# Kernel tuning notes

Measured on AMD Instinct MI355X. Metric: run time of the kernel, lower is better.

## Reference

```python
import jax, jax.numpy as jnp
import numpy as np

B, T, V, D, H, L, NFF, K = 16, 256, 30000, 512, 256, 2, 2, 20
# D = input_size = hidden_size (required by residual in FeedForwardNet); H = hidden_size//2 per LSTM direction


def _lstm_dir(x, Wih, Whh, b, reverse):
    # x: [B,T,Din]; Wih: [4H,Din]; Whh: [4H,H]; b: [4H] (b_ih + b_hh)
    Bq = x.shape[0]
    Hd = Whh.shape[1]
    if reverse:
        x = x[:, ::-1]
    xw = jnp.einsum('bti,gi->btg', x, Wih) + b  # [B,T,4H]

    def step(carry, xw_t):
        h, c = carry
        g = xw_t + h @ Whh.T
        i, f, gg, o = jnp.split(g, 4, axis=-1)  # torch gate order i,f,g,o
        c = jax.nn.sigmoid(f) * c + jax.nn.sigmoid(i) * jnp.tanh(gg)
        h = jax.nn.sigmoid(o) * jnp.tanh(c)
        return (h, c), h

    h0 = jnp.zeros((Bq, Hd), x.dtype)
    _, hs = jax.lax.scan(step, (h0, h0), jnp.swapaxes(xw, 0, 1))
    hs = jnp.swapaxes(hs, 0, 1)  # [B,T,H]
    if reverse:
        hs = hs[:, ::-1]
    return hs


def _bilstm(x, Wih, Whh, b):
    # Wih: [L,2,4H,Din], Whh: [L,2,4H,H], b: [L,2,4H]; Din = 2H = D for all layers
    h = x
    for l in range(L):
        fwd = _lstm_dir(h, Wih[l, 0], Whh[l, 0], b[l, 0], False)
        bwd = _lstm_dir(h, Wih[l, 1], Whh[l, 1], b[l, 1], True)
        h = jnp.concatenate([fwd, bwd], axis=-1)  # [B,T,2H]
    return h


def _viterbi(em, start, end, trans):
    # em: [B,T,K] emissions, full mask; torchcrf Viterbi decode
    Bq, Tq, Kq = em.shape
    score = start + em[:, 0]  # [B,K]

    def step(score, em_t):
        bs = score[:, :, None] + trans[None] + em_t[:, None, :]  # [B,K,K]
        return jnp.max(bs, axis=1), jnp.argmax(bs, axis=1)

    score, hist = jax.lax.scan(step, score, jnp.swapaxes(em[:, 1:], 0, 1))  # hist [T-1,B,K]
    best = jnp.argmax(score + end, axis=-1)  # [B]

    def back(tag, h_t):
        prev = jnp.take_along_axis(h_t, tag[:, None], axis=1)[:, 0]
        return prev, prev

    _, prevs = jax.lax.scan(back, best, hist, reverse=True)  # [T-1,B]
    return jnp.concatenate([prevs, best[None]], axis=0).T  # [B,T]


def setup_inputs() -> dict:
    key = jax.random.key(0)
    ks = jax.random.split(key, 16)
    s = 0.05
    inp = {
        'x': jax.random.randint(ks[0], (B, T), 0, V),
        'emb': jax.random.normal(ks[1], (V, D), jnp.float32) * s,
        'lstm_Wih': jax.random.normal(ks[2], (L, 2, 4 * H, D), jnp.float32) * s,
        'lstm_Whh': jax.random.normal(ks[3], (L, 2, 4 * H, H), jnp.float32) * s,
        'lstm_b': jax.random.normal(ks[4], (L, 2, 4 * H), jnp.float32) * s,
        'ff_W1': jax.random.normal(ks[5], (NFF, D, D), jnp.float32) * s,
        'ff_b1': jax.random.normal(ks[6], (NFF, D), jnp.float32) * s,
        'ff_W2': jax.random.normal(ks[7], (NFF, D, D), jnp.float32) * s,
        'ff_b2': jax.random.normal(ks[8], (NFF, D), jnp.float32) * s,
        'ffo_W': jax.random.normal(ks[9], (H, D), jnp.float32) * s,
        'ffo_b': jax.random.normal(ks[10], (H,), jnp.float32) * s,
        'out_W': jax.random.normal(ks[11], (K, H), jnp.float32) * s,
        'out_b': jax.random.normal(ks[12], (K,), jnp.float32) * s,
        'crf_start': jax.random.normal(ks[13], (K,), jnp.float32) * 0.1,
        'crf_end': jax.random.normal(ks[14], (K,), jnp.float32) * 0.1,
        'crf_trans': jax.random.normal(ks[15], (K, K), jnp.float32) * 0.1,
    }
    return inp


def reference(x, emb, lstm_Wih, lstm_Whh, lstm_b, ff_W1, ff_b1, ff_W2, ff_b2,
              ffo_W, ffo_b, out_W, out_b, crf_start, crf_end, crf_trans):
    h = emb[x]                       # [B,T,D] frozen embedding lookup
    h = _bilstm(h, lstm_Wih, lstm_Whh, lstm_b)  # [B,T,D] (2H == D)
    res = h
    for n in range(NFF):             # residual MLP stack (dropout = identity in eval)
        h = jax.nn.relu(h @ ff_W1[n].T + ff_b1[n]) @ ff_W2[n].T + ff_b2[n]
    h = h + res
    h = h @ ffo_W.T + ffo_b          # [B,T,H] FeedForwardNet.output
    em = h @ out_W.T + out_b         # [B,T,K] emissions
    tag = _viterbi(em, crf_start, crf_end, crf_trans)  # [B,T] int32
    return em, tag
```

## Files before the change

kernel.cpp:

```cpp
#include <hip/hip_runtime.h>
#include <hip/hip_bf16.h>
#include <stdint.h>

typedef unsigned short u16;
typedef unsigned int   u32;
typedef __attribute__((ext_vector_type(4))) float f32x4;
typedef __attribute__((ext_vector_type(8))) short bf16x8;

static __device__ __forceinline__ u16 f2bf(float x) {
  union { float f; u32 u; } v; v.f = x;
  u32 r = v.u + 0x7FFFu + ((v.u >> 16) & 1u);
  return (u16)(r >> 16);
}
static __device__ __forceinline__ float bf2f(u16 b) {
  union { u32 u; float f; } v; v.u = ((u32)b) << 16;
  return v.f;
}


__global__ void split_hl(const float* __restrict__ in, u16* __restrict__ hi,
                         u16* __restrict__ lo, int n) {
  int i = blockIdx.x * 256 + threadIdx.x;
  if (i < n) {
    float v = in[i];
    u16 h = f2bf(v);
    hi[i] = h;
    lo[i] = f2bf(v - bf2f(h));
  }
}

__global__ void embed_split(const int* __restrict__ x, const float* __restrict__ emb,
                            u16* __restrict__ hi, u16* __restrict__ lo) {
  int gid = blockIdx.x * 256 + threadIdx.x;
  int bt = gid >> 9, d = gid & 511;
  float v = emb[(size_t)x[bt] * 512 + d];
  u16 h = f2bf(v);
  hi[gid] = h;
  lo[gid] = f2bf(v - bf2f(h));
}

__global__ void lstm_wpack(const float* __restrict__ Whh, u32* __restrict__ wp) {
  int tid = blockIdx.x * 256 + threadIdx.x;
  int dw   = tid & 3;
  int lane = (tid >> 2) & 63;
  int kt   = (tid >> 8) & 7;
  int g    = (tid >> 11) & 3;
  int W    = (tid >> 13) & 15;
  int d    = (tid >> 17) & 1;
  int lyr  = (tid >> 18) & 1;
  int row = g * 256 + W * 16 + (lane & 15);
  int k   = kt * 32 + (lane >> 4) * 8 + dw * 2;
  const float* src = Whh + (((size_t)(lyr * 2 + d) * 1024 + row) * 256);
  u16 h0 = f2bf(src[k]), h1 = f2bf(src[k + 1]);
  wp[tid] = (u32)h0 | ((u32)h1 << 16);
}

__global__ void resadd_split(const float* __restrict__ a, const float* __restrict__ b,
                             u16* __restrict__ hi, u16* __restrict__ lo, int n) {
  int i = blockIdx.x * 256 + threadIdx.x;
  if (i < n) {
    float v = a[i] + b[i];
    u16 h = f2bf(v);
    hi[i] = h;
    lo[i] = f2bf(v - bf2f(h));
  }
}

template<int RELU, int WF32, int WHL, int XSWZ, int BLO>
__global__ __launch_bounds__(256) void gemm_x3(
    const u16* __restrict__ Ahi, const u16* __restrict__ Alo,
    const u16* __restrict__ Bhi, const u16* __restrict__ Blo,
    const float* __restrict__ bias,
    float* __restrict__ Cf, u16* __restrict__ Chi, u16* __restrict__ Clo,
    int M, int N, int Kd)
{
  __shared__ u16 As_hi[128][40], As_lo[128][40], Bs_hi[128][40];
  __shared__ u16 Bs_lo[BLO ? 128 : 1][BLO ? 40 : 1];
  int t = threadIdx.x;
  int bm = blockIdx.x * 128, bn = blockIdx.y * 128;
  int l = t & 63, wid = t >> 6;
  int wy = wid >> 1, wx = wid & 1;
  f32x4 acc[4][4];
#pragma unroll
  for (int i = 0; i < 4; i++)
#pragma unroll
    for (int j = 0; j < 4; j++) acc[i][j] = (f32x4){0.f, 0.f, 0.f, 0.f};

  for (int kt = 0; kt < Kd; kt += 32) {
    __syncthreads();
#pragma unroll
    for (int cc = 0; cc < 2; cc++) {
      int c = t + cc * 256;
      int row = c >> 2, k8 = (c & 3) << 3;
      *(uint4*)&As_hi[row][k8] = *(const uint4*)(Ahi + (size_t)(bm + row) * Kd + kt + k8);
      *(uint4*)&As_lo[row][k8] = *(const uint4*)(Alo + (size_t)(bm + row) * Kd + kt + k8);
      *(uint4*)&Bs_hi[row][k8] = *(const uint4*)(Bhi + (size_t)(bn + row) * Kd + kt + k8);
      if (BLO)
        *(uint4*)&Bs_lo[row][k8] = *(const uint4*)(Blo + (size_t)(bn + row) * Kd + kt + k8);
    }
    __syncthreads();
    bf16x8 bh[4], bl[4];
    int k8 = (l >> 4) << 3;
#pragma unroll
    for (int ni = 0; ni < 4; ni++) {
      int r = wx * 64 + ni * 16 + (l & 15);
      bh[ni] = *(const bf16x8*)&Bs_hi[r][k8];
      if (BLO) bl[ni] = *(const bf16x8*)&Bs_lo[r][k8];
    }
#pragma unroll
    for (int mi = 0; mi < 4; mi++) {
      int r = wy * 64 + mi * 16 + (l & 15);
      bf16x8 ah = *(const bf16x8*)&As_hi[r][k8];
      bf16x8 al = *(const bf16x8*)&As_lo[r][k8];
#pragma unroll
      for (int ni = 0; ni < 4; ni++) {
        acc[mi][ni] = __builtin_amdgcn_mfma_f32_16x16x32_bf16(ah, bh[ni], acc[mi][ni], 0, 0, 0);
        acc[mi][ni] = __builtin_amdgcn_mfma_f32_16x16x32_bf16(al, bh[ni], acc[mi][ni], 0, 0, 0);
        if (BLO)
          acc[mi][ni] = __builtin_amdgcn_mfma_f32_16x16x32_bf16(ah, bl[ni], acc[mi][ni], 0, 0, 0);
      }
    }
  }
#pragma unroll
  for (int ni = 0; ni < 4; ni++) {
    int col = bn + wx * 64 + ni * 16 + (l & 15);
    float bv = bias ? bias[col] : 0.f;
#pragma unroll
    for (int mi = 0; mi < 4; mi++) {
#pragma unroll
      for (int r = 0; r < 4; r++) {
        int row = bm + wy * 64 + mi * 16 + (l >> 4) * 4 + r;
        float v = acc[mi][ni][r] + bv;
        if (RELU) v = fmaxf(v, 0.f);
        if (XSWZ) {
          int tt = row & 255, b = row >> 8;
          int g = col >> 8, c8 = col & 255;
          int Wv = c8 >> 4, uu = c8 & 15;
          int lane = ((b >> 2) << 4) | uu;
          size_t o = ((((size_t)tt * 16 + Wv) * 4 + g) * 64 + lane) * 4 + (b & 3);
          Cf[o] = v;
        } else {
          size_t o = (size_t)row * N + col;
          if (WF32) Cf[o] = v;
          if (WHL) { u16 h = f2bf(v); Chi[o] = h; Clo[o] = f2bf(v - bf2f(h)); }
        }
      }
    }
  }
}

__global__ __launch_bounds__(1024, 1) void lstm_rec3(
    const u32* __restrict__ wpack_l,
    const float* __restrict__ xwsw_f, const float* __restrict__ xwsw_b,
    u16* __restrict__ out_hi, u16* __restrict__ out_lo, float* __restrict__ out_f)
{
  int dir = blockIdx.x;
  int tid = threadIdx.x;
  int W = tid >> 6, l = tid & 63;
  int bb  = l & 15;
  int mb  = (l >> 4) * 4;
  int wu  = W * 16 + (l & 15);
  const float* xw = dir ? xwsw_b : xwsw_f;

  bf16x8 wf[4][8];
#pragma unroll
  for (int g = 0; g < 4; g++) {
    const u32* wb = wpack_l + (size_t)((dir * 16 + W) * 4 + g) * 2048;
#pragma unroll
    for (int kt = 0; kt < 8; kt++)
      wf[g][kt] = *(const bf16x8*)(const void*)(wb + (kt * 64 + l) * 4);
  }

  __shared__ u16 hH[2][16][256];

  f32x4 cst = (f32x4){0.f, 0.f, 0.f, 0.f};

  for (int s = 0; s < 256; s++) {
    int tpos = dir ? (255 - s) : s;
    int cb = s & 1, pb = cb ^ 1;

    const float* xb = xw + ((size_t)tpos * 16 + W) * 1024;
    f32x4 xwv[4];
#pragma unroll
    for (int g = 0; g < 4; g++)
      xwv[g] = *(const f32x4*)(xb + g * 256 + l * 4);

    f32x4 acc[4];
#pragma unroll
    for (int g = 0; g < 4; g++) acc[g] = (f32x4){0.f, 0.f, 0.f, 0.f};

    if (s > 0) {
#pragma unroll
      for (int kt = 0; kt < 8; kt++) {
        int bx = (((kt * 4 + (l >> 4)) ^ (bb & 7)) << 3);
        bf16x8 ah = *(const bf16x8*)&hH[pb][bb][bx];
#pragma unroll
        for (int g = 0; g < 4; g++)
          acc[g] = __builtin_amdgcn_mfma_f32_16x16x32_bf16(ah, wf[g][kt], acc[g], 0, 0, 0);
      }
    }

#pragma unroll
    for (int r = 0; r < 4; r++) {
      float gi = acc[0][r] + xwv[0][r];
      float gf = acc[1][r] + xwv[1][r];
      float gg = acc[2][r] + xwv[2][r];
      float go = acc[3][r] + xwv[3][r];
      float si = 1.f / (1.f + __expf(-gi));
      float sf = 1.f / (1.f + __expf(-gf));
      float so = 1.f / (1.f + __expf(-go));
      float tg = 1.f - 2.f / (__expf(2.f * gg) + 1.f);
      float c = sf * cst[r] + si * tg;
      cst[r] = c;
      float th = 1.f - 2.f / (__expf(2.f * c) + 1.f);
      float h = so * th;

      u16 hb = f2bf(h);
      u16 lb = f2bf(h - bf2f(hb));
      int b = mb + r;
      int idx = ((((wu >> 3) ^ (b & 7)) << 3)) + (wu & 7);
      hH[cb][b][idx] = hb;
      size_t oo = (((size_t)b * 256 + tpos) * 512) + dir * 256 + wu;
      out_hi[oo] = hb;
      out_lo[oo] = lb;
      if (out_f) out_f[oo] = h;
    }
    __syncthreads();
  }
}

__global__ __launch_bounds__(256) void out_gemm(const float* __restrict__ h,
                                                const float* __restrict__ Wo,
                                                const float* __restrict__ bo,
                                                float* __restrict__ em)
{
  int t = threadIdx.x;
  if (t >= 160) return;
  int r = t / 20, j = t - r * 20;
  int bt = blockIdx.x * 8 + r;
  const float* hr = h + (size_t)bt * 256;
  const float* wr = Wo + j * 256;
  float acc = 0.f;
#pragma unroll 4
  for (int k = 0; k < 256; k++) acc += hr[k] * wr[k];
  em[(size_t)bt * 20 + j] = acc + bo[j];
}

__global__ __launch_bounds__(192) void viterbi(const float* __restrict__ em,
                                               const float* __restrict__ cstart,
                                               const float* __restrict__ cend,
                                               const float* __restrict__ ctrans,
                                               float* __restrict__ tago)
{
  __shared__ float sc[8][20];
  __shared__ float tl[400];
  __shared__ unsigned char hist[255][8][20];
  int t = threadIdx.x;
  for (int i = t; i < 400; i += 192) tl[i] = ctrans[i];
  int bl = t / 20, j = t - bl * 20;
  bool act = (t < 160);
  int b = blockIdx.x * 8 + bl;
  if (act) sc[bl][j] = cstart[j] + em[((size_t)b * 256) * 20 + j];
  __syncthreads();
  for (int step = 1; step < 256; step++) {
    float best = -1e30f; int bi = 0;
    if (act) {
      best = sc[bl][0] + tl[j]; bi = 0;
#pragma unroll
      for (int i = 1; i < 20; i++) {
        float v = sc[bl][i] + tl[i * 20 + j];
        if (v > best) { best = v; bi = i; }
      }
      hist[step - 1][bl][j] = (unsigned char)bi;
    }
    __syncthreads();
    if (act) sc[bl][j] = best + em[((size_t)b * 256 + step) * 20 + j];
    __syncthreads();
  }
  if (act && j == 0) {
    float best = sc[bl][0] + cend[0]; int bj = 0;
    for (int i = 1; i < 20; i++) {
      float v = sc[bl][i] + cend[i];
      if (v > best) { best = v; bj = i; }
    }
    int tag = bj;
    tago[(size_t)b * 256 + 255] = (float)tag;
    for (int step = 254; step >= 0; step--) {
      tag = hist[step][bl][tag];
      tago[(size_t)b * 256 + step] = (float)tag;
    }
  }
}

extern "C" void kernel_launch(void* const* d_in, const int* in_sizes, int n_in,
                              void* d_out, int out_size, void* d_ws, size_t ws_size,
                              hipStream_t stream)
{
  const int*   x   = (const int*)  d_in[0];
  const float* emb = (const float*)d_in[1];
  const float* Wih = (const float*)d_in[2];
  const float* Whh = (const float*)d_in[3];
  const float* lb  = (const float*)d_in[4];
  const float* fW1 = (const float*)d_in[5];
  const float* fb1 = (const float*)d_in[6];
  const float* fW2 = (const float*)d_in[7];
  const float* fb2 = (const float*)d_in[8];
  const float* foW = (const float*)d_in[9];
  const float* fob = (const float*)d_in[10];
  const float* oW  = (const float*)d_in[11];
  const float* ob  = (const float*)d_in[12];
  const float* cst = (const float*)d_in[13];
  const float* cen = (const float*)d_in[14];
  const float* ctr = (const float*)d_in[15];

  const size_t MB = 1u << 20;
  if (ws_size < 100 * MB) return;
  char* ws = (char*)d_ws;

  u16* embHi = (u16*)(ws + 0 * MB);
  u16* embLo = (u16*)(ws + 4 * MB);
  u16* l1Hi  = (u16*)(ws + 8 * MB);
  u16* l1Lo  = (u16*)(ws + 12 * MB);
  float* l2F = (float*)(ws + 16 * MB);
  u16* l2Hi  = (u16*)(ws + 24 * MB);
  u16* l2Lo  = (u16*)(ws + 28 * MB);
  float* xwF = (float*)(ws + 32 * MB);
  float* xwB = (float*)(ws + 48 * MB);
  u32* wpck  = (u32*)(ws + 80 * MB);
  u16* wihHi = (u16*)(ws + 84 * MB);
  u16* wihLo = (u16*)(ws + 88 * MB);
  u16* fw1Hi = (u16*)(ws + 92 * MB);
  u16* fw1Lo = (u16*)(ws + 93 * MB);
  u16* fw2Hi = (u16*)(ws + 94 * MB);
  u16* fw2Lo = (u16*)(ws + 95 * MB);
  u16* ffoHi = (u16*)(ws + 96 * MB);
  u16* ffoLo = (u16*)(ws + 96 * MB + 512 * 1024);
  u16* t1Hi = (u16*)xwF;
  u16* t1Lo = (u16*)((char*)xwF + 4 * MB);
  u16* t2Hi = (u16*)xwB;
  u16* t2Lo = (u16*)((char*)xwB + 4 * MB);
  float* h2F = (float*)((char*)xwB + 8 * MB);
  u16* sumHi = (u16*)((char*)xwF + 8 * MB);
  u16* sumLo = (u16*)((char*)xwF + 12 * MB);
  float* h256F = (float*)xwF;

  float* em   = (float*)d_out;
  float* tago = (float*)d_out + 81920;

  dim3 blk(256);

  split_hl<<<8192, blk, 0, stream>>>(Wih, wihHi, wihLo, 4 * 1024 * 512);
  split_hl<<<2048, blk, 0, stream>>>(fW1, fw1Hi, fw1Lo, 2 * 512 * 512);
  split_hl<<<2048, blk, 0, stream>>>(fW2, fw2Hi, fw2Lo, 2 * 512 * 512);
  split_hl<<<512,  blk, 0, stream>>>(foW, ffoHi, ffoLo, 256 * 512);
  lstm_wpack<<<2048, blk, 0, stream>>>(Whh, wpck);
  embed_split<<<8192, blk, 0, stream>>>(x, emb, embHi, embLo);

  gemm_x3<0,1,0,1,0><<<dim3(32, 8), blk, 0, stream>>>(embHi, embLo,
      wihHi + 0 * 524288, wihLo + 0 * 524288, lb + 0 * 1024,
      xwF, nullptr, nullptr, 4096, 1024, 512);
  gemm_x3<0,1,0,1,0><<<dim3(32, 8), blk, 0, stream>>>(embHi, embLo,
      wihHi + 1 * 524288, wihLo + 1 * 524288, lb + 1 * 1024,
      xwB, nullptr, nullptr, 4096, 1024, 512);
  lstm_rec3<<<2, dim3(1024), 0, stream>>>(wpck, xwF, xwB, l1Hi, l1Lo, nullptr);

  gemm_x3<0,1,0,1,0><<<dim3(32, 8), blk, 0, stream>>>(l1Hi, l1Lo,
      wihHi + 2 * 524288, wihLo + 2 * 524288, lb + 2 * 1024,
      xwF, nullptr, nullptr, 4096, 1024, 512);
  gemm_x3<0,1,0,1,0><<<dim3(32, 8), blk, 0, stream>>>(l1Hi, l1Lo,
      wihHi + 3 * 524288, wihLo + 3 * 524288, lb + 3 * 1024,
      xwB, nullptr, nullptr, 4096, 1024, 512);
  lstm_rec3<<<2, dim3(1024), 0, stream>>>(wpck + 262144, xwF, xwB,
      l2Hi, l2Lo, l2F);

  gemm_x3<1,0,1,0,0><<<dim3(32, 4), blk, 0, stream>>>(l2Hi, l2Lo,
      fw1Hi + 0, fw1Lo + 0, fb1 + 0, nullptr, t1Hi, t1Lo, 4096, 512, 512);
  gemm_x3<0,0,1,0,0><<<dim3(32, 4), blk, 0, stream>>>(t1Hi, t1Lo,
      fw2Hi + 0, fw2Lo + 0, fb2 + 0, nullptr, t2Hi, t2Lo, 4096, 512, 512);
  gemm_x3<1,0,1,0,0><<<dim3(32, 4), blk, 0, stream>>>(t2Hi, t2Lo,
      fw1Hi + 262144, fw1Lo + 262144, fb1 + 512, nullptr, t1Hi, t1Lo, 4096, 512, 512);
  gemm_x3<0,1,0,0,0><<<dim3(32, 4), blk, 0, stream>>>(t1Hi, t1Lo,
      fw2Hi + 262144, fw2Lo + 262144, fb2 + 512, h2F, nullptr, nullptr, 4096, 512, 512);
  resadd_split<<<8192, blk, 0, stream>>>(h2F, l2F, sumHi, sumLo, 4096 * 512);
  gemm_x3<0,1,0,0,0><<<dim3(32, 2), blk, 0, stream>>>(sumHi, sumLo,
      ffoHi, ffoLo, fob, h256F, nullptr, nullptr, 4096, 256, 512);

  out_gemm<<<512, blk, 0, stream>>>(h256F, oW, ob, em);
  viterbi<<<2, dim3(192), 0, stream>>>(em, cst, cen, ctr, tago);
}
```

Measured before the change: 6.236 ms.

## Run LSTM recurrence in fp8 with a two-pass bf16 weight-residual correction

The recurrent matmul now uses fp8 MFMA with fp8-packed Whh held in registers, and 512-thread blocks each cover 32 hidden units. A first pass runs the recurrence to get approximate h. A parallel bf16 GEMM then multiplies those h values by the fp8 quantization residual of Whh, and a second fp8 pass adds that correction and also carries an fp8 hi/lo split of h. The aim is to shorten the serial per-step critical path. In exchange each layer runs the recurrence twice plus extra GEMMs, and accuracy depends on the correction from the first-pass h being close enough.

```diff
diff --git a/kernel.cpp b/kernel.cpp
--- a/kernel.cpp
+++ b/kernel.cpp
@@ -6,6 +6,7 @@
 typedef unsigned int   u32;
 typedef __attribute__((ext_vector_type(4))) float f32x4;
 typedef __attribute__((ext_vector_type(8))) short bf16x8;
+typedef __attribute__((ext_vector_type(4))) unsigned short u16x4;
 
 static __device__ __forceinline__ u16 f2bf(float x) {
   union { float f; u32 u; } v; v.f = x;
@@ -39,42 +40,53 @@
   lo[gid] = f2bf(v - bf2f(h));
 }
 
-__global__ void lstm_wpack(const float* __restrict__ Whh, u32* __restrict__ wp) {
+__global__ void lstm_wpack_fp8(const float* __restrict__ Whh, u32* __restrict__ wp,
+                               u16* __restrict__ dW) {
   int tid = blockIdx.x * 256 + threadIdx.x;
-  int dw   = tid & 3;
-  int lane = (tid >> 2) & 63;
-  int kt   = (tid >> 8) & 7;
+  int dw   = tid & 1;
+  int lane = (tid >> 1) & 63;
+  int kt   = (tid >> 7) & 7;
+  int ni   = (tid >> 10) & 1;
   int g    = (tid >> 11) & 3;
-  int W    = (tid >> 13) & 15;
-  int d    = (tid >> 17) & 1;
-  int lyr  = (tid >> 18) & 1;
-  int row = g * 256 + W * 16 + (lane & 15);
-  int k   = kt * 32 + (lane >> 4) * 8 + dw * 2;
-  const float* src = Whh + (((size_t)(lyr * 2 + d) * 1024 + row) * 256);
-  u16 h0 = f2bf(src[k]), h1 = f2bf(src[k + 1]);
-  wp[tid] = (u32)h0 | ((u32)h1 << 16);
-}
-
-__global__ void resadd_split(const float* __restrict__ a, const float* __restrict__ b,
+  int W    = (tid >> 13) & 7;
+  int dir  = (tid >> 16) & 1;
+  int lyr  = (tid >> 17) & 1;
+  int row = g * 256 + W * 32 + ni * 16 + (lane & 15);
+  int k   = kt * 32 + (lane >> 4) * 8 + dw * 4;
+  int ld = lyr * 2 + dir;
+  const float* src = Whh + (((size_t)ld * 1024 + row) * 256);
+  u32 v = __builtin_amdgcn_cvt_pk_fp8_f32(src[k], src[k + 1], 0, 0);
+  v = __builtin_amdgcn_cvt_pk_fp8_f32(src[k + 2], src[k + 3], v, 1);
+  wp[tid] = v;
+  u16* dst = dW + ((size_t)ld * 1024 + row) * 256 + k;
+  dst[0] = f2bf(src[k]     - __builtin_amdgcn_cvt_f32_fp8((int)v, 0));
+  dst[1] = f2bf(src[k + 1] - __builtin_amdgcn_cvt_f32_fp8((int)v, 1));
+  dst[2] = f2bf(src[k + 2] - __builtin_amdgcn_cvt_f32_fp8((int)v, 2));
+  dst[3] = f2bf(src[k + 3] - __builtin_amdgcn_cvt_f32_fp8((int)v, 3));
+}
+
+__global__ void resadd_split(const float* __restrict__ a, const u16* __restrict__ bHi,
+                             const u16* __restrict__ bLo,
                              u16* __restrict__ hi, u16* __restrict__ lo, int n) {
   int i = blockIdx.x * 256 + threadIdx.x;
   if (i < n) {
-    float v = a[i] + b[i];
+    float v = a[i] + bf2f(bHi[i]) + bf2f(bLo[i]);
     u16 h = f2bf(v);
     hi[i] = h;
     lo[i] = f2bf(v - bf2f(h));
   }
 }
 
-template<int RELU, int WF32, int WHL, int XSWZ, int BLO>
+template<int RELU, int WF32, int WHL, int XSWZ, int BLO, int ALO>
 __global__ __launch_bounds__(256) void gemm_x3(
     const u16* __restrict__ Ahi, const u16* __restrict__ Alo,
     const u16* __restrict__ Bhi, const u16* __restrict__ Blo,
     const float* __restrict__ bias,
     float* __restrict__ Cf, u16* __restrict__ Chi, u16* __restrict__ Clo,
-    int M, int N, int Kd)
+    int M, int N, int Kd, int lda)
 {
-  __shared__ u16 As_hi[128][40], As_lo[128][40], Bs_hi[128][40];
+  __shared__ u16 As_hi[128][40], Bs_hi[128][40];
+  __shared__ u16 As_lo[ALO ? 128 : 1][ALO ? 40 : 1];
   __shared__ u16 Bs_lo[BLO ? 128 : 1][BLO ? 40 : 1];
   int t = threadIdx.x;
   int bm = blockIdx.x * 128, bn = blockIdx.y * 128;
@@ -92,8 +104,9 @@
     for (int cc = 0; cc < 2; cc++) {
       int c = t + cc * 256;
       int row = c >> 2, k8 = (c & 3) << 3;
-      *(uint4*)&As_hi[row][k8] = *(const uint4*)(Ahi + (size_t)(bm + row) * Kd + kt + k8);
-      *(uint4*)&As_lo[row][k8] = *(const uint4*)(Alo + (size_t)(bm + row) * Kd + kt + k8);
+      *(uint4*)&As_hi[row][k8] = *(const uint4*)(Ahi + (size_t)(bm + row) * lda + kt + k8);
+      if (ALO)
+        *(uint4*)&As_lo[row][k8] = *(const uint4*)(Alo + (size_t)(bm + row) * lda + kt + k8);
       *(uint4*)&Bs_hi[row][k8] = *(const uint4*)(Bhi + (size_t)(bn + row) * Kd + kt + k8);
       if (BLO)
         *(uint4*)&Bs_lo[row][k8] = *(const uint4*)(Blo + (size_t)(bn + row) * Kd + kt + k8);
@@ -111,11 +124,13 @@
     for (int mi = 0; mi < 4; mi++) {
       int r = wy * 64 + mi * 16 + (l & 15);
       bf16x8 ah = *(const bf16x8*)&As_hi[r][k8];
-      bf16x8 al = *(const bf16x8*)&As_lo[r][k8];
+      bf16x8 al;
+      if (ALO) al = *(const bf16x8*)&As_lo[r][k8];
 #pragma unroll
       for (int ni = 0; ni < 4; ni++) {
         acc[mi][ni] = __builtin_amdgcn_mfma_f32_16x16x32_bf16(ah, bh[ni], acc[mi][ni], 0, 0, 0);
-        acc[mi][ni] = __builtin_amdgcn_mfma_f32_16x16x32_bf16(al, bh[ni], acc[mi][ni], 0, 0, 0);
+        if (ALO)
+          acc[mi][ni] = __builtin_amdgcn_mfma_f32_16x16x32_bf16(al, bh[ni], acc[mi][ni], 0, 0, 0);
         if (BLO)
           acc[mi][ni] = __builtin_amdgcn_mfma_f32_16x16x32_bf16(ah, bl[ni], acc[mi][ni], 0, 0, 0);
       }
@@ -134,11 +149,12 @@
         if (RELU) v = fmaxf(v, 0.f);
         if (XSWZ) {
           int tt = row & 255, b = row >> 8;
-          int g = col >> 8, c8 = col & 255;
-          int Wv = c8 >> 4, uu = c8 & 15;
+          int g = col >> 8, u8 = col & 255;
+          int Wv = u8 >> 5, nn = (u8 >> 4) & 1, uu = u8 & 15;
           int lane = ((b >> 2) << 4) | uu;
-          size_t o = ((((size_t)tt * 16 + Wv) * 4 + g) * 64 + lane) * 4 + (b & 3);
-          Cf[o] = v;
+          size_t o = ((((((size_t)tt * 8 + Wv) * 4 + g) * 2 + nn) * 64) + lane) * 4 + (b & 3);
+          if (WHL) Chi[o] = f2bf(v);
+          else Cf[o] = v;
         } else {
           size_t o = (size_t)row * N + col;
           if (WF32) Cf[o] = v;
@@ -149,81 +165,122 @@
   }
 }
 
-__global__ __launch_bounds__(1024, 1) void lstm_rec3(
+template<int PASS>
+__global__ __launch_bounds__(512, 2) void lstm_rec5(
     const u32* __restrict__ wpack_l,
     const float* __restrict__ xwsw_f, const float* __restrict__ xwsw_b,
-    u16* __restrict__ out_hi, u16* __restrict__ out_lo, float* __restrict__ out_f)
+    const u16* __restrict__ corr_f, const u16* __restrict__ corr_b,
+    u16* __restrict__ h1out,
+    u16* __restrict__ out_hi, u16* __restrict__ out_lo)
 {
   int dir = blockIdx.x;
   int tid = threadIdx.x;
   int W = tid >> 6, l = tid & 63;
   int bb  = l & 15;
   int mb  = (l >> 4) * 4;
-  int wu  = W * 16 + (l & 15);
   const float* xw = dir ? xwsw_b : xwsw_f;
-
-  bf16x8 wf[4][8];
-#pragma unroll
-  for (int g = 0; g < 4; g++) {
-    const u32* wb = wpack_l + (size_t)((dir * 16 + W) * 4 + g) * 2048;
-#pragma unroll
-    for (int kt = 0; kt < 8; kt++)
-      wf[g][kt] = *(const bf16x8*)(const void*)(wb + (kt * 64 + l) * 4);
-  }
-
-  __shared__ u16 hH[2][16][256];
-
-  f32x4 cst = (f32x4){0.f, 0.f, 0.f, 0.f};
+  const u16* corr = dir ? corr_b : corr_f;
+
+  long wf[4][2][8];
+  {
+    const long* wp64 = (const long*)wpack_l;
+#pragma unroll
+    for (int g = 0; g < 4; g++)
+#pragma unroll
+      for (int ni = 0; ni < 2; ni++)
+#pragma unroll
+        for (int kt = 0; kt < 8; kt++)
+          wf[g][ni][kt] = wp64[(size_t)((((dir * 8 + W) * 4 + g) * 2 + ni) * 8 + kt) * 64 + l];
+  }
+
+  __shared__ unsigned char hH8[2][16][256];
+  __shared__ unsigned char hL8[PASS == 2 ? 2 : 1][PASS == 2 ? 16 : 1][PASS == 2 ? 256 : 1];
+
+  f32x4 cst[2] = {(f32x4){0.f,0.f,0.f,0.f}, (f32x4){0.f,0.f,0.f,0.f}};
 
   for (int s = 0; s < 256; s++) {
     int tpos = dir ? (255 - s) : s;
     int cb = s & 1, pb = cb ^ 1;
 
-    const float* xb = xw + ((size_t)tpos * 16 + W) * 1024;
-    f32x4 xwv[4];
+    const float* xb = xw + ((size_t)tpos * 8 + W) * 2048;
+    f32x4 acc[4][2];
 #pragma unroll
     for (int g = 0; g < 4; g++)
-      xwv[g] = *(const f32x4*)(xb + g * 256 + l * 4);
-
-    f32x4 acc[4];
-#pragma unroll
-    for (int g = 0; g < 4; g++) acc[g] = (f32x4){0.f, 0.f, 0.f, 0.f};
+#pragma unroll
+      for (int ni = 0; ni < 2; ni++)
+        acc[g][ni] = *(const f32x4*)(xb + (g * 2 + ni) * 256 + l * 4);
+
+    if (PASS == 2 && s > 0) {
+      int tprev = dir ? (tpos + 1) : (tpos - 1);
+      const u16* cbp = corr + ((size_t)tprev * 8 + W) * 2048;
+#pragma unroll
+      for (int g = 0; g < 4; g++)
+#pragma unroll
+        for (int ni = 0; ni < 2; ni++) {
+          u16x4 cv = *(const u16x4*)(cbp + (g * 2 + ni) * 256 + l * 4);
+#pragma unroll
+          for (int r = 0; r < 4; r++) acc[g][ni][r] += bf2f(cv[r]);
+        }
+    }
 
     if (s > 0) {
 #pragma unroll
       for (int kt = 0; kt < 8; kt++) {
-        int bx = (((kt * 4 + (l >> 4)) ^ (bb & 7)) << 3);
-        bf16x8 ah = *(const bf16x8*)&hH[pb][bb][bx];
+        int off = (((kt * 4 + (l >> 4)) ^ (bb & 7)) << 3);
+        long ah = *(const long*)&hH8[pb][bb][off];
 #pragma unroll
         for (int g = 0; g < 4; g++)
-          acc[g] = __builtin_amdgcn_mfma_f32_16x16x32_bf16(ah, wf[g][kt], acc[g], 0, 0, 0);
+#pragma unroll
+          for (int ni = 0; ni < 2; ni++)
+            acc[g][ni] = __builtin_amdgcn_mfma_f32_16x16x32_fp8_fp8(ah, wf[g][ni][kt], acc[g][ni], 0, 0, 0);
+        if (PASS == 2) {
+          long al = *(const long*)&hL8[pb][bb][off];
+#pragma unroll
+          for (int g = 0; g < 4; g++)
+#pragma unroll
+            for (int ni = 0; ni < 2; ni++)
+              acc[g][ni] = __builtin_amdgcn_mfma_f32_16x16x32_fp8_fp8(al, wf[g][ni][kt], acc[g][ni], 0, 0, 0);
+        }
       }
     }
 
 #pragma unroll
-    for (int r = 0; r < 4; r++) {
-      float gi = acc[0][r] + xwv[0][r];
-      float gf = acc[1][r] + xwv[1][r];
-      float gg = acc[2][r] + xwv[2][r];
-      float go = acc[3][r] + xwv[3][r];
-      float si = 1.f / (1.f + __expf(-gi));
-      float sf = 1.f / (1.f + __expf(-gf));
-      float so = 1.f / (1.f + __expf(-go));
-      float tg = 1.f - 2.f / (__expf(2.f * gg) + 1.f);
-      float c = sf * cst[r] + si * tg;
-      cst[r] = c;
-      float th = 1.f - 2.f / (__expf(2.f * c) + 1.f);
-      float h = so * th;
-
-      u16 hb = f2bf(h);
-      u16 lb = f2bf(h - bf2f(hb));
-      int b = mb + r;
-      int idx = ((((wu >> 3) ^ (b & 7)) << 3)) + (wu & 7);
-      hH[cb][b][idx] = hb;
-      size_t oo = (((size_t)b * 256 + tpos) * 512) + dir * 256 + wu;
-      out_hi[oo] = hb;
-      out_lo[oo] = lb;
-      if (out_f) out_f[oo] = h;
+    for (int ni = 0; ni < 2; ni++) {
+      int u = W * 32 + ni * 16 + (l & 15);
+#pragma unroll
+      for (int r = 0; r < 4; r++) {
+        float gi = acc[0][ni][r];
+        float gf = acc[1][ni][r];
+        float gg = acc[2][ni][r];
+        float go = acc[3][ni][r];
+        float si = 1.f / (1.f + __expf(-gi));
+        float sf = 1.f / (1.f + __expf(-gf));
+        float so = 1.f / (1.f + __expf(-go));
+        float tg = 1.f - 2.f / (__expf(2.f * gg) + 1.f);
+        float c = sf * cst[ni][r] + si * tg;
+        cst[ni][r] = c;
+        float th = 1.f - 2.f / (__expf(2.f * c) + 1.f);
+        float h = so * th;
+
+        int b = mb + r;
+        int idx = (((u >> 3) ^ (b & 7)) << 3) + (u & 7);
+        u32 ph = __builtin_amdgcn_cvt_pk_fp8_f32(h, h, 0, 0);
+        hH8[cb][b][idx] = (unsigned char)(ph & 0xFF);
+        if (PASS == 2) {
+          float fh = __builtin_amdgcn_cvt_f32_fp8((int)ph, 0);
+          u32 pl = __builtin_amdgcn_cvt_pk_fp8_f32(h - fh, h - fh, 0, 0);
+          hL8[cb][b][idx] = (unsigned char)(pl & 0xFF);
+        }
+
+        size_t oo = (((size_t)b * 256 + tpos) * 512) + dir * 256 + u;
+        if (PASS == 1) {
+          h1out[oo] = f2bf(h);
+        } else {
+          u16 hb = f2bf(h);
+          out_hi[oo] = hb;
+          out_lo[oo] = f2bf(h - bf2f(hb));
+        }
+      }
     }
     __syncthreads();
   }
@@ -314,27 +371,30 @@
   const float* ctr = (const float*)d_in[15];
 
   const size_t MB = 1u << 20;
-  if (ws_size < 100 * MB) return;
+  if (ws_size < 95 * MB) return;
   char* ws = (char*)d_ws;
 
   u16* embHi = (u16*)(ws + 0 * MB);
   u16* embLo = (u16*)(ws + 4 * MB);
   u16* l1Hi  = (u16*)(ws + 8 * MB);
   u16* l1Lo  = (u16*)(ws + 12 * MB);
-  float* l2F = (float*)(ws + 16 * MB);
-  u16* l2Hi  = (u16*)(ws + 24 * MB);
-  u16* l2Lo  = (u16*)(ws + 28 * MB);
-  float* xwF = (float*)(ws + 32 * MB);
-  float* xwB = (float*)(ws + 48 * MB);
-  u32* wpck  = (u32*)(ws + 80 * MB);
-  u16* wihHi = (u16*)(ws + 84 * MB);
-  u16* wihLo = (u16*)(ws + 88 * MB);
-  u16* fw1Hi = (u16*)(ws + 92 * MB);
-  u16* fw1Lo = (u16*)(ws + 93 * MB);
-  u16* fw2Hi = (u16*)(ws + 94 * MB);
-  u16* fw2Lo = (u16*)(ws + 95 * MB);
-  u16* ffoHi = (u16*)(ws + 96 * MB);
-  u16* ffoLo = (u16*)(ws + 96 * MB + 512 * 1024);
+  u16* l2Hi  = (u16*)(ws + 16 * MB);
+  u16* l2Lo  = (u16*)(ws + 20 * MB);
+  float* xwF = (float*)(ws + 24 * MB);
+  float* xwB = (float*)(ws + 40 * MB);
+  u16* corrF = (u16*)(ws + 56 * MB);
+  u16* corrB = (u16*)(ws + 64 * MB);
+  u16* h1    = (u16*)(ws + 72 * MB);
+  u32* wpck  = (u32*)(ws + 76 * MB);
+  u16* dW    = (u16*)(ws + 77 * MB);
+  u16* wihHi = (u16*)(ws + 79 * MB);
+  u16* wihLo = (u16*)(ws + 83 * MB);
+  u16* fw1Hi = (u16*)(ws + 87 * MB);
+  u16* fw1Lo = (u16*)(ws + 88 * MB);
+  u16* fw2Hi = (u16*)(ws + 89 * MB);
+  u16* fw2Lo = (u16*)(ws + 90 * MB);
+  u16* ffoHi = (u16*)(ws + 91 * MB);
+  u16* ffoLo = (u16*)(ws + 91 * MB + 512 * 1024);
   u16* t1Hi = (u16*)xwF;
   u16* t1Lo = (u16*)((char*)xwF + 4 * MB);
   u16* t2Hi = (u16*)xwB;
@@ -353,37 +413,48 @@
   split_hl<<<2048, blk, 0, stream>>>(fW1, fw1Hi, fw1Lo, 2 * 512 * 512);
   split_hl<<<2048, blk, 0, stream>>>(fW2, fw2Hi, fw2Lo, 2 * 512 * 512);
   split_hl<<<512,  blk, 0, stream>>>(foW, ffoHi, ffoLo, 256 * 512);
-  lstm_wpack<<<2048, blk, 0, stream>>>(Whh, wpck);
+  lstm_wpack_fp8<<<1024, blk, 0, stream>>>(Whh, wpck, dW);
   embed_split<<<8192, blk, 0, stream>>>(x, emb, embHi, embLo);
 
-  gemm_x3<0,1,0,1,0><<<dim3(32, 8), blk, 0, stream>>>(embHi, embLo,
-      wihHi + 0 * 524288, wihLo + 0 * 524288, lb + 0 * 1024,
-      xwF, nullptr, nullptr, 4096, 1024, 512);
-  gemm_x3<0,1,0,1,0><<<dim3(32, 8), blk, 0, stream>>>(embHi, embLo,
-      wihHi + 1 * 524288, wihLo + 1 * 524288, lb + 1 * 1024,
-      xwB, nullptr, nullptr, 4096, 1024, 512);
-  lstm_rec3<<<2, dim3(1024), 0, stream>>>(wpck, xwF, xwB, l1Hi, l1Lo, nullptr);
-
-  gemm_x3<0,1,0,1,0><<<dim3(32, 8), blk, 0, stream>>>(l1Hi, l1Lo,
-      wihHi + 2 * 524288, wihLo + 2 * 524288, lb + 2 * 1024,
-      xwF, nullptr, nullptr, 4096, 1024, 512);
-  gemm_x3<0,1,0,1,0><<<dim3(32, 8), blk, 0, stream>>>(l1Hi, l1Lo,
-      wihHi + 3 * 524288, wihLo + 3 * 524288, lb + 3 * 1024,
-      xwB, nullptr, nullptr, 4096, 1024, 512);
-  lstm_rec3<<<2, dim3(1024), 0, stream>>>(wpck + 262144, xwF, xwB,
-      l2Hi, l2Lo, l2F);
-
-  gemm_x3<1,0,1,0,0><<<dim3(32, 4), blk, 0, stream>>>(l2Hi, l2Lo,
-      fw1Hi + 0, fw1Lo + 0, fb1 + 0, nullptr, t1Hi, t1Lo, 4096, 512, 512);
-  gemm_x3<0,0,1,0,0><<<dim3(32, 4), blk, 0, stream>>>(t1Hi, t1Lo,
-      fw2Hi + 0, fw2Lo + 0, fb2 + 0, nullptr, t2Hi, t2Lo, 4096, 512, 512);
-  gemm_x3<1,0,1,0,0><<<dim3(32, 4), blk, 0, stream>>>(t2Hi, t2Lo,
-      fw1Hi + 262144, fw1Lo + 262144, fb1 + 512, nullptr, t1Hi, t1Lo, 4096, 512, 512);
-  gemm_x3<0,1,0,0,0><<<dim3(32, 4), blk, 0, stream>>>(t1Hi, t1Lo,
-      fw2Hi + 262144, fw2Lo + 262144, fb2 + 512, h2F, nullptr, nullptr, 4096, 512, 512);
-  resadd_split<<<8192, blk, 0, stream>>>(h2F, l2F, sumHi, sumLo, 4096 * 512);
-  gemm_x3<0,1,0,0,0><<<dim3(32, 2), blk, 0, stream>>>(sumHi, sumLo,
-      ffoHi, ffoLo, fob, h256F, nullptr, nullptr, 4096, 256, 512);
+  for (int lyr = 0; lyr < 2; lyr++) {
+    const u16* inHi = lyr ? l1Hi : embHi;
+    const u16* inLo = lyr ? l1Lo : embLo;
+    u16* outHi = lyr ? l2Hi : l1Hi;
+    u16* outLo = lyr ? l2Lo : l1Lo;
+    const u32* wp_l = wpck + lyr * 131072;
+
+    gemm_x3<0,1,0,1,0,1><<<dim3(32, 8), blk, 0, stream>>>(inHi, inLo,
+        wihHi + (lyr * 2 + 0) * 524288, wihLo + (lyr * 2 + 0) * 524288,
+        lb + (lyr * 2 + 0) * 1024, xwF, nullptr, nullptr, 4096, 1024, 512, 512);
+    gemm_x3<0,1,0,1,0,1><<<dim3(32, 8), blk, 0, stream>>>(inHi, inLo,
+        wihHi + (lyr * 2 + 1) * 524288, wihLo + (lyr * 2 + 1) * 524288,
+        lb + (lyr * 2 + 1) * 1024, xwB, nullptr, nullptr, 4096, 1024, 512, 512);
+
+    lstm_rec5<1><<<2, dim3(512), 0, stream>>>(wp_l, xwF, xwB,
+        nullptr, nullptr, h1, nullptr, nullptr);
+
+    gemm_x3<0,0,1,1,0,0><<<dim3(32, 8), blk, 0, stream>>>(h1 + 0, h1,
+        dW + (size_t)(lyr * 2 + 0) * 262144, nullptr, nullptr,
+        nullptr, corrF, nullptr, 4096, 1024, 256, 512);
+    gemm_x3<0,0,1,1,0,0><<<dim3(32, 8), blk, 0, stream>>>(h1 + 256, h1,
+        dW + (size_t)(lyr * 2 + 1) * 262144, nullptr, nullptr,
+        nullptr, corrB, nullptr, 4096, 1024, 256, 512);
+
+    lstm_rec5<2><<<2, dim3(512), 0, stream>>>(wp_l, xwF, xwB,
+        corrF, corrB, nullptr, outHi, outLo);
+  }
+
+  gemm_x3<1,0,1,0,0,1><<<dim3(32, 4), blk, 0, stream>>>(l2Hi, l2Lo,
+      fw1Hi + 0, fw1Lo + 0, fb1 + 0, nullptr, t1Hi, t1Lo, 4096, 512, 512, 512);
+  gemm_x3<0,0,1,0,0,1><<<dim3(32, 4), blk, 0, stream>>>(t1Hi, t1Lo,
+      fw2Hi + 0, fw2Lo + 0, fb2 + 0, nullptr, t2Hi, t2Lo, 4096, 512, 512, 512);
+  gemm_x3<1,0,1,0,0,1><<<dim3(32, 4), blk, 0, stream>>>(t2Hi, t2Lo,
+      fw1Hi + 262144, fw1Lo + 262144, fb1 + 512, nullptr, t1Hi, t1Lo, 4096, 512, 512, 512);
+  gemm_x3<0,1,0,0,0,1><<<dim3(32, 4), blk, 0, stream>>>(t1Hi, t1Lo,
+      fw2Hi + 262144, fw2Lo + 262144, fb2 + 512, h2F, nullptr, nullptr, 4096, 512, 512, 512);
+  resadd_split<<<8192, blk, 0, stream>>>(h2F, l2Hi, l2Lo, sumHi, sumLo, 4096 * 512);
+  gemm_x3<0,1,0,0,0,1><<<dim3(32, 2), blk, 0, stream>>>(sumHi, sumLo,
+      ffoHi, ffoLo, fob, h256F, nullptr, nullptr, 4096, 256, 512, 512);
 
   out_gemm<<<512, blk, 0, stream>>>(h256F, oW, ob, em);
   viterbi<<<2, dim3(192), 0, stream>>>(em, cst, cen, ctr, tago);
```

Measured after the change: 5.446 ms. -12.7%, faster.
